# Optimization experiments

Measured on AMD Instinct MI355X. Metric: run time of the kernel, lower is better.

The kernel has to match this reference:

```python
import jax, jax.numpy as jnp
import numpy as np

B, C, H, W = 16, 512, 32, 32
G = 32            # GroupNorm groups (hard-coded in Normalize)
EPS = 1e-6
TEXT = 180        # text_ch
F = H * W         # in_features, asserted H*W == in_features


def setup_inputs() -> dict:
    key = jax.random.key(0)
    ks = jax.random.split(key, 10)
    s = 0.02
    return {
        "x": jax.random.normal(ks[0], (B, C, H, W), dtype=jnp.float32),
        "condition": jax.random.normal(ks[1], (B, TEXT), dtype=jnp.float32),
        "gamma": jnp.ones((C,), dtype=jnp.float32),
        "beta": jnp.zeros((C,), dtype=jnp.float32),
        "wq": jax.random.normal(ks[2], (C, C), dtype=jnp.float32) * s,   # 1x1 conv [out,in]
        "bq": jax.random.normal(ks[3], (C,), dtype=jnp.float32) * s,
        "wk": jax.random.normal(ks[4], (F, TEXT), dtype=jnp.float32) * s,  # Linear(text_ch -> in_features)
        "bk": jax.random.normal(ks[5], (F,), dtype=jnp.float32) * s,
        "wv": jax.random.normal(ks[6], (F, TEXT), dtype=jnp.float32) * s,
        "bv": jax.random.normal(ks[7], (F,), dtype=jnp.float32) * s,
        "wo": jax.random.normal(ks[8], (C, C), dtype=jnp.float32) * s,   # proj_out 1x1 conv
        "bo": jax.random.normal(ks[9], (C,), dtype=jnp.float32) * s,
    }


def _group_norm(x, gamma, beta):
    b, c, h, w = x.shape
    xg = x.reshape(b, G, c // G, h, w)
    mu = xg.mean(axis=(2, 3, 4), keepdims=True)
    var = xg.var(axis=(2, 3, 4), keepdims=True)
    xn = ((xg - mu) * jax.lax.rsqrt(var + EPS)).reshape(b, c, h, w)
    return xn * gamma[None, :, None, None] + beta[None, :, None, None]


def reference(x, condition, gamma, beta, wq, bq, wk, bk, wv, bv, wo, bo):
    h_ = _group_norm(x, gamma, beta)                       # [B,C,H,W]
    # q: 1x1 conv
    q = jnp.einsum('bchw,oc->bohw', h_, wq) + bq[None, :, None, None]
    # condition.reshape(B,1,-1).repeat(1,C,1)
    cond = jnp.broadcast_to(condition[:, None, :], (B, C, TEXT))  # [B,C,T]
    k = jnp.einsum('bct,ft->bcf', cond, wk) + bk           # [B,C,F]
    v = jnp.einsum('bct,ft->bcf', cond, wv) + bv           # [B,C,F]
    q3 = q.reshape(B, C, H * W).transpose(0, 2, 1)         # [B,N,C], N=HW
    scale = C ** (-0.5)
    attn = jax.nn.softmax(jnp.einsum('bnc,bcf->bnf', q3, k) * scale, axis=2)  # [B,N,F]
    h2 = jnp.einsum('bcf,bnf->bcn', v, attn).reshape(B, C, H, W)
    out = jnp.einsum('bchw,oc->bohw', h2, wo) + bo[None, :, None, None]
    return x + out
```

## Files before the change

### kernel.cpp

```cpp
#include <hip/hip_runtime.h>

#define B_   16
#define C_   512
#define N_   1024
#define F_   1024
#define T_   180
#define G_   32

#define WS_MU    0
#define WS_RSIG  512
#define WS_K     1024
#define WS_V     (1024 + 16384)
#define WS_WQS   (1024 + 2*16384)
#define WS_WOS   (WS_WQS + 512)
#define WS_BQS   (WS_WOS + 512)
#define WS_POFF  (WS_BQS + 4)
#define WS_P     36864

__global__ __launch_bounds__(256) void k_w(
    const float* __restrict__ cond,
    const float* __restrict__ wq, const float* __restrict__ bq,
    const float* __restrict__ wk, const float* __restrict__ bk,
    const float* __restrict__ wv, const float* __restrict__ bv,
    const float* __restrict__ wo, float* __restrict__ ws)
{
    const int blk = blockIdx.x;
    const int tid = threadIdx.x;

    if (blk < 16) {
        const int c0 = blk << 5;
        const int oi = tid >> 5;
        const int ci = tid & 31;
        float acc = 0.f;
        #pragma unroll 8
        for (int ob = 0; ob < 64; ++ob) {
            const int o = (ob << 3) + oi;
            acc += wq[o * C_ + c0 + ci];
        }
        __shared__ float part[8][32];
        part[oi][ci] = acc;
        __syncthreads();
        if (tid < 32) {
            float s = 0.f;
            #pragma unroll
            for (int j = 0; j < 8; ++j) s += part[j][tid];
            ws[WS_WQS + c0 + tid] = s;
        }
    } else if (blk < 32) {
        const int o0 = (blk - 16) << 5;
        const int r  = tid >> 3;
        const int j  = tid & 7;
        const float4* row = (const float4*)(wo + (size_t)(o0 + r) * C_);
        float acc = 0.f;
        #pragma unroll
        for (int jj = 0; jj < 16; ++jj) {
            float4 p = row[(jj << 3) + j];
            acc += (p.x + p.y) + (p.z + p.w);
        }
        #pragma unroll
        for (int off = 4; off; off >>= 1) acc += __shfl_down(acc, off, 8);
        if (j == 0) ws[WS_WOS + o0 + r] = acc;
    } else if (blk < 96) {
        const int idx = blk - 32;
        const int b   = idx >> 2;
        const int f   = ((idx & 3) << 8) + tid;
        __shared__ __align__(16) float condl[T_];
        if (tid < T_) condl[tid] = cond[b * T_ + tid];
        __syncthreads();
        const float4* c4  = (const float4*)condl;
        const float4* wk4 = (const float4*)(wk + (size_t)f * T_);
        const float4* wv4 = (const float4*)(wv + (size_t)f * T_);
        float accK = bk[f];
        float accV = bv[f];
        #pragma unroll 5
        for (int t4 = 0; t4 < 45; ++t4) {
            float4 cf = c4[t4];
            float4 a  = wk4[t4];
            float4 vv = wv4[t4];
            accK = fmaf(cf.x, a.x,  fmaf(cf.y, a.y,  fmaf(cf.z, a.z,  fmaf(cf.w, a.w,  accK))));
            accV = fmaf(cf.x, vv.x, fmaf(cf.y, vv.y, fmaf(cf.z, vv.z, fmaf(cf.w, vv.w, accV))));
        }
        ws[WS_K + b * F_ + f] = accK;
        ws[WS_V + b * F_ + f] = accV;
    } else {
        float p = bq[tid] + bq[tid + 256];
        #pragma unroll
        for (int off = 32; off; off >>= 1) p += __shfl_down(p, off, 64);
        __shared__ float rb[4];
        if ((tid & 63) == 0) rb[tid >> 6] = p;
        __syncthreads();
        if (tid == 0) ws[WS_BQS] = rb[0] + rb[1] + rb[2] + rb[3];
    }
}

__global__ __launch_bounds__(256) void k_stats(
    const float* __restrict__ x, const float* __restrict__ gamma,
    const float* __restrict__ beta, float* __restrict__ ws)
{
    const int blk = blockIdx.x;
    const int g   = blk & 31;
    const int tid = threadIdx.x;

    __shared__ float wl[16], bwl[16];
    __shared__ float rs[4], rq[4];
    if (tid < 16) {
        const int c = (g << 4) + tid;
        const float wqs = ws[WS_WQS + c];
        wl[tid]  = gamma[c] * wqs;
        bwl[tid] = beta[c]  * wqs;
    }
    __syncthreads();

    const float4* xv = (const float4*)(x + (size_t)blk * 16384);
    float4 p4 = make_float4(0.f, 0.f, 0.f, 0.f);
    float s = 0.f, sq = 0.f;
    #pragma unroll
    for (int j = 0; j < 16; ++j) {
        float4 p = xv[tid + (j << 8)];
        s  += (p.x + p.y) + (p.z + p.w);
        sq += p.x * p.x + p.y * p.y + p.z * p.z + p.w * p.w;
        const float wj = wl[j];
        p4.x = fmaf(p.x, wj, p4.x);
        p4.y = fmaf(p.y, wj, p4.y);
        p4.z = fmaf(p.z, wj, p4.z);
        p4.w = fmaf(p.w, wj, p4.w);
    }
    *(float4*)(ws + WS_P + (size_t)blk * 1024 + (tid << 2)) = p4;

    #pragma unroll
    for (int off = 32; off; off >>= 1) {
        s  += __shfl_down(s,  off, 64);
        sq += __shfl_down(sq, off, 64);
    }
    if ((tid & 63) == 0) { rs[tid >> 6] = s; rq[tid >> 6] = sq; }
    __syncthreads();
    if (tid == 0) {
        const float S1 = rs[0] + rs[1] + rs[2] + rs[3];
        const float S2 = rq[0] + rq[1] + rq[2] + rq[3];
        const float mu  = S1 * (1.f / 16384.f);
        const float var = S2 * (1.f / 16384.f) - mu * mu;
        const float rsig = rsqrtf(var + 1e-6f);
        ws[WS_MU   + blk] = mu;
        ws[WS_RSIG + blk] = rsig;
        float sw = 0.f, sbw = 0.f;
        #pragma unroll
        for (int j = 0; j < 16; ++j) { sw += wl[j]; sbw += bwl[j]; }
        ws[WS_POFF + blk] = sbw - mu * rsig * sw;
    }
}

__global__ __launch_bounds__(256) void k_fused(
    const float* __restrict__ x, const float* __restrict__ bo,
    const float* __restrict__ ws, float* __restrict__ out)
{
    const int b   = blockIdx.x >> 5;
    const int n0  = (blockIdx.x & 31) << 5;
    const int tid = threadIdx.x;

    __shared__ __align__(16) float KV[2 * F_];
    __shared__ float rsigl[32];
    __shared__ float part[8][32];
    __shared__ float pse[8][32], psv[8][32];
    __shared__ float Sl[32], Al[32];
    __shared__ float redmx[4], redmn[4];
    __shared__ float opw;

    if (tid < 32) rsigl[tid] = ws[WS_RSIG + (b << 5) + tid];
    float op = (tid < 32) ? ws[WS_POFF + (b << 5) + tid] : 0.f;

    const float* Kg = ws + WS_K + b * F_;
    const float* Vg = ws + WS_V + b * F_;
    float mx = -1e30f, mn = 1e30f;
    float2* KV2 = (float2*)KV;
    #pragma unroll
    for (int i = tid; i < F_; i += 256) {
        float kv = Kg[i];
        KV2[i] = make_float2(kv, Vg[i]);
        mx = fmaxf(mx, kv);
        mn = fminf(mn, kv);
    }
    #pragma unroll
    for (int off = 32; off; off >>= 1) {
        op += __shfl_down(op, off, 64);
        mx = fmaxf(mx, __shfl_down(mx, off, 64));
        mn = fminf(mn, __shfl_down(mn, off, 64));
    }
    if ((tid & 63) == 0) {
        redmx[tid >> 6] = mx;
        redmn[tid >> 6] = mn;
        if (tid == 0) opw = op + ws[WS_BQS];
    }
    __syncthreads();
    const float offset = opw;
    const float maxK = fmaxf(fmaxf(redmx[0], redmx[1]), fmaxf(redmx[2], redmx[3]));
    const float minK = fminf(fminf(redmn[0], redmn[1]), fminf(redmn[2], redmn[3]));

    const int nl = tid & 31;
    const int gq = tid >> 5;
    {
        const float* Pp = ws + WS_P + ((size_t)((b << 5) + (gq << 2)) << 10) + n0 + nl;
        float acc = 0.f;
        #pragma unroll
        for (int j = 0; j < 4; ++j)
            acc = fmaf(rsigl[(gq << 2) + j], Pp[(size_t)j << 10], acc);
        part[gq][nl] = acc;
    }
    __syncthreads();
    if (tid < 32) {
        float s8 = 0.f;
        #pragma unroll
        for (int j = 0; j < 8; ++j) s8 += part[j][tid];
        Sl[tid] = s8 + offset;
    }
    __syncthreads();

    const float LOG2E = 1.4426950408889634f;
    const float scale = 0.044194173824159216f;
    const float s  = Sl[nl] * scale;
    const float sl = s * LOG2E;
    const float ml = (s >= 0.f ? maxK : minK) * sl;

    float se = 0.f, sv = 0.f;
    const int fq = tid >> 5;
    const int fbase = fq << 7;
    #pragma unroll 8
    for (int fi = 0; fi < 128; ++fi) {
        float2 kv = KV2[fbase + fi];
        float e = exp2f(fmaf(sl, kv.x, -ml));
        se += e;
        sv = fmaf(kv.y, e, sv);
    }
    pse[fq][nl] = se;
    psv[fq][nl] = sv;

    const int col = tid & 7;
    const int row = tid >> 3;
    const float* WOS = ws + WS_WOS;
    float wv_[16], bo_[16];
    #pragma unroll
    for (int p = 0; p < 16; ++p) {
        wv_[p] = WOS[(p << 5) + row];
        bo_[p] = bo[(p << 5) + row];
    }

    __syncthreads();
    if (tid < 32) {
        float den = 0.f, num = 0.f;
        #pragma unroll
        for (int j = 0; j < 8; ++j) { den += pse[j][tid]; num += psv[j][tid]; }
        Al[tid] = num / den;
    }
    __syncthreads();

    float av[4];
    #pragma unroll
    for (int j = 0; j < 4; ++j) av[j] = Al[(col << 2) + j];

    #pragma unroll
    for (int p = 0; p < 16; ++p) {
        const int o = (p << 5) + row;
        const size_t base = (((size_t)(b * C_ + o)) << 10) + n0 + (col << 2);
        float4 xv = *(const float4*)(x + base);
        float4 ov;
        ov.x = xv.x + fmaf(av[0], wv_[p], bo_[p]);
        ov.y = xv.y + fmaf(av[1], wv_[p], bo_[p]);
        ov.z = xv.z + fmaf(av[2], wv_[p], bo_[p]);
        ov.w = xv.w + fmaf(av[3], wv_[p], bo_[p]);
        *(float4*)(out + base) = ov;
    }
}

extern "C" void kernel_launch(void* const* d_in, const int* in_sizes, int n_in,
                              void* d_out, int out_size, void* d_ws, size_t ws_size,
                              hipStream_t stream) {
    const float* x     = (const float*)d_in[0];
    const float* cond  = (const float*)d_in[1];
    const float* gamma = (const float*)d_in[2];
    const float* beta  = (const float*)d_in[3];
    const float* wq    = (const float*)d_in[4];
    const float* bq    = (const float*)d_in[5];
    const float* wk    = (const float*)d_in[6];
    const float* bk    = (const float*)d_in[7];
    const float* wv    = (const float*)d_in[8];
    const float* bv    = (const float*)d_in[9];
    const float* wo    = (const float*)d_in[10];
    const float* bo    = (const float*)d_in[11];
    float* ws  = (float*)d_ws;
    float* out = (float*)d_out;

    hipLaunchKernelGGL(k_w, dim3(97), dim3(256), 0, stream,
                       cond, wq, bq, wk, bk, wv, bv, wo, ws);
    hipLaunchKernelGGL(k_stats, dim3(512), dim3(256), 0, stream,
                       x, gamma, beta, ws);
    hipLaunchKernelGGL(k_fused, dim3(512), dim3(256), 0, stream,
                       x, bo, ws, out);
}
```

Baseline: 125.9 us.

## Split fused attention kernel into attention-scalar kernel and streaming output kernel

The fused kernel is split in two. k_attn computes the per-position attention scalar A and writes it to workspace. A new k_out kernel then does the x + A*wo + bo residual as a grid-stride float4 stream over 2048 blocks. The aim is to decouple the memory-bound output pass from the exp-heavy attention part, giving better occupancy and coalesced streaming. In exchange it adds a kernel launch and a small workspace round-trip, and moves the WS_P offset.

```diff
diff --git a/kernel.cpp b/kernel.cpp
--- a/kernel.cpp
+++ b/kernel.cpp
@@ -15,7 +15,8 @@
 #define WS_WOS   (WS_WQS + 512)
 #define WS_BQS   (WS_WOS + 512)
 #define WS_POFF  (WS_BQS + 4)
-#define WS_P     36864
+#define WS_A     (WS_POFF + 512)
+#define WS_P     65536
 
 __global__ __launch_bounds__(256) void k_w(
     const float* __restrict__ cond,
@@ -149,10 +150,10 @@
     }
 }
 
-__global__ __launch_bounds__(256) void k_fused(
-    const float* __restrict__ x, const float* __restrict__ bo,
-    const float* __restrict__ ws, float* __restrict__ out)
-{
+__global__ __launch_bounds__(256) void k_attn(
+    const float* __restrict__ ws_in, float* __restrict__ ws)
+{
+    const float* wsr = ws_in;
     const int b   = blockIdx.x >> 5;
     const int n0  = (blockIdx.x & 31) << 5;
     const int tid = threadIdx.x;
@@ -161,15 +162,15 @@
     __shared__ float rsigl[32];
     __shared__ float part[8][32];
     __shared__ float pse[8][32], psv[8][32];
-    __shared__ float Sl[32], Al[32];
+    __shared__ float Sl[32];
     __shared__ float redmx[4], redmn[4];
     __shared__ float opw;
 
-    if (tid < 32) rsigl[tid] = ws[WS_RSIG + (b << 5) + tid];
-    float op = (tid < 32) ? ws[WS_POFF + (b << 5) + tid] : 0.f;
-
-    const float* Kg = ws + WS_K + b * F_;
-    const float* Vg = ws + WS_V + b * F_;
+    if (tid < 32) rsigl[tid] = wsr[WS_RSIG + (b << 5) + tid];
+    float op = (tid < 32) ? wsr[WS_POFF + (b << 5) + tid] : 0.f;
+
+    const float* Kg = wsr + WS_K + b * F_;
+    const float* Vg = wsr + WS_V + b * F_;
     float mx = -1e30f, mn = 1e30f;
     float2* KV2 = (float2*)KV;
     #pragma unroll
@@ -188,7 +189,7 @@
     if ((tid & 63) == 0) {
         redmx[tid >> 6] = mx;
         redmn[tid >> 6] = mn;
-        if (tid == 0) opw = op + ws[WS_BQS];
+        if (tid == 0) opw = op + wsr[WS_BQS];
     }
     __syncthreads();
     const float offset = opw;
@@ -198,7 +199,7 @@
     const int nl = tid & 31;
     const int gq = tid >> 5;
     {
-        const float* Pp = ws + WS_P + ((size_t)((b << 5) + (gq << 2)) << 10) + n0 + nl;
+        const float* Pp = wsr + WS_P + ((size_t)((b << 5) + (gq << 2)) << 10) + n0 + nl;
         float acc = 0.f;
         #pragma unroll
         for (int j = 0; j < 4; ++j)
@@ -232,41 +233,37 @@
     }
     pse[fq][nl] = se;
     psv[fq][nl] = sv;
-
-    const int col = tid & 7;
-    const int row = tid >> 3;
-    const float* WOS = ws + WS_WOS;
-    float wv_[16], bo_[16];
-    #pragma unroll
-    for (int p = 0; p < 16; ++p) {
-        wv_[p] = WOS[(p << 5) + row];
-        bo_[p] = bo[(p << 5) + row];
-    }
-
     __syncthreads();
     if (tid < 32) {
         float den = 0.f, num = 0.f;
         #pragma unroll
         for (int j = 0; j < 8; ++j) { den += pse[j][tid]; num += psv[j][tid]; }
-        Al[tid] = num / den;
-    }
-    __syncthreads();
-
-    float av[4];
-    #pragma unroll
-    for (int j = 0; j < 4; ++j) av[j] = Al[(col << 2) + j];
-
-    #pragma unroll
-    for (int p = 0; p < 16; ++p) {
-        const int o = (p << 5) + row;
-        const size_t base = (((size_t)(b * C_ + o)) << 10) + n0 + (col << 2);
-        float4 xv = *(const float4*)(x + base);
+        ws[WS_A + (b << 10) + n0 + tid] = num / den;
+    }
+}
+
+__global__ __launch_bounds__(256) void k_out(
+    const float* __restrict__ x, const float* __restrict__ bo,
+    const float* __restrict__ ws, float* __restrict__ out)
+{
+    const int tot4 = B_ * C_ * (N_ / 4);
+    const int stride = 2048 * 256;
+    int i4 = blockIdx.x * 256 + threadIdx.x;
+    #pragma unroll 4
+    for (int it = 0; it < 4; ++it, i4 += stride) {
+        const int n4 = i4 & 255;
+        const int o  = (i4 >> 8) & 511;
+        const int b  = i4 >> 17;
+        const float4 a4 = *(const float4*)(ws + WS_A + (b << 10) + (n4 << 2));
+        const float w   = ws[WS_WOS + o];
+        const float bof = bo[o];
+        const float4 xv = ((const float4*)x)[i4];
         float4 ov;
-        ov.x = xv.x + fmaf(av[0], wv_[p], bo_[p]);
-        ov.y = xv.y + fmaf(av[1], wv_[p], bo_[p]);
-        ov.z = xv.z + fmaf(av[2], wv_[p], bo_[p]);
-        ov.w = xv.w + fmaf(av[3], wv_[p], bo_[p]);
-        *(float4*)(out + base) = ov;
+        ov.x = xv.x + fmaf(a4.x, w, bof);
+        ov.y = xv.y + fmaf(a4.y, w, bof);
+        ov.z = xv.z + fmaf(a4.z, w, bof);
+        ov.w = xv.w + fmaf(a4.w, w, bof);
+        ((float4*)out)[i4] = ov;
     }
 }
 
@@ -292,6 +289,8 @@
                        cond, wq, bq, wk, bk, wv, bv, wo, ws);
     hipLaunchKernelGGL(k_stats, dim3(512), dim3(256), 0, stream,
                        x, gamma, beta, ws);
-    hipLaunchKernelGGL(k_fused, dim3(512), dim3(256), 0, stream,
+    hipLaunchKernelGGL(k_attn, dim3(512), dim3(256), 0, stream,
+                       ws, ws);
+    hipLaunchKernelGGL(k_out, dim3(2048), dim3(256), 0, stream,
                        x, bo, ws, out);
 }
```

Result: slower. 131.7 us (+4.6%).

## Merge weight-prep and group-stats kernels into one prep kernel

Applied to the files above, without the earlier changes.

Fuses the weight-reduction kernel and the GroupNorm statistics kernel into a single launch. Each stats block now recomputes the wq column sums for its own 16 channels instead of reading them from a prior kernel, and it issues its x loads into registers before that reduction so the two overlap. This removes one kernel launch and the dependency gap between the two. In exchange, the wq column-sum work is repeated across the 16 batches, and register pressure rises from holding 16 float4 values per thread.

```diff
diff --git a/kernel.cpp b/kernel.cpp
--- a/kernel.cpp
+++ b/kernel.cpp
@@ -11,14 +11,14 @@
 #define WS_RSIG  512
 #define WS_K     1024
 #define WS_V     (1024 + 16384)
-#define WS_WQS   (1024 + 2*16384)
-#define WS_WOS   (WS_WQS + 512)
+#define WS_WOS   (1024 + 2*16384)
 #define WS_BQS   (WS_WOS + 512)
 #define WS_POFF  (WS_BQS + 4)
 #define WS_P     36864
 
-__global__ __launch_bounds__(256) void k_w(
-    const float* __restrict__ cond,
+__global__ __launch_bounds__(256) void k_prep(
+    const float* __restrict__ x, const float* __restrict__ gamma,
+    const float* __restrict__ beta, const float* __restrict__ cond,
     const float* __restrict__ wq, const float* __restrict__ bq,
     const float* __restrict__ wk, const float* __restrict__ bk,
     const float* __restrict__ wv, const float* __restrict__ bv,
@@ -27,41 +27,76 @@
     const int blk = blockIdx.x;
     const int tid = threadIdx.x;
 
-    if (blk < 16) {
-        const int c0 = blk << 5;
-        const int oi = tid >> 5;
-        const int ci = tid & 31;
-        float acc = 0.f;
-        #pragma unroll 8
-        for (int ob = 0; ob < 64; ++ob) {
-            const int o = (ob << 3) + oi;
-            acc += wq[o * C_ + c0 + ci];
-        }
-        __shared__ float part[8][32];
-        part[oi][ci] = acc;
-        __syncthreads();
-        if (tid < 32) {
-            float s = 0.f;
+    if (blk < 512) {
+        const int g  = blk & 31;
+        const int c0 = g << 4;
+
+        const float4* xv = (const float4*)(x + (size_t)blk * 16384);
+        float4 xr[16];
+        #pragma unroll
+        for (int j = 0; j < 16; ++j) xr[j] = xv[tid + (j << 8)];
+
+        __shared__ float wqpart[16][16];
+        {
+            const int j  = tid & 15;
+            const int oi = tid >> 4;
+            const float* wqp = wq + (size_t)oi * C_ + c0 + j;
+            float a = 0.f;
+            #pragma unroll 8
+            for (int k = 0; k < 32; ++k)
+                a += wqp[(size_t)(k << 4) * C_];
+            wqpart[oi][j] = a;
+        }
+        __syncthreads();
+        __shared__ float wl[16], bwl[16];
+        if (tid < 16) {
+            float wqs = 0.f;
             #pragma unroll
-            for (int j = 0; j < 8; ++j) s += part[j][tid];
-            ws[WS_WQS + c0 + tid] = s;
-        }
-    } else if (blk < 32) {
-        const int o0 = (blk - 16) << 5;
-        const int r  = tid >> 3;
-        const int j  = tid & 7;
-        const float4* row = (const float4*)(wo + (size_t)(o0 + r) * C_);
-        float acc = 0.f;
-        #pragma unroll
-        for (int jj = 0; jj < 16; ++jj) {
-            float4 p = row[(jj << 3) + j];
-            acc += (p.x + p.y) + (p.z + p.w);
-        }
-        #pragma unroll
-        for (int off = 4; off; off >>= 1) acc += __shfl_down(acc, off, 8);
-        if (j == 0) ws[WS_WOS + o0 + r] = acc;
-    } else if (blk < 96) {
-        const int idx = blk - 32;
+            for (int k = 0; k < 16; ++k) wqs += wqpart[k][tid];
+            const int c = c0 + tid;
+            wl[tid]  = gamma[c] * wqs;
+            bwl[tid] = beta[c]  * wqs;
+        }
+        __syncthreads();
+
+        float4 p4 = make_float4(0.f, 0.f, 0.f, 0.f);
+        float s = 0.f, sq = 0.f;
+        #pragma unroll
+        for (int j = 0; j < 16; ++j) {
+            float4 p = xr[j];
+            s  += (p.x + p.y) + (p.z + p.w);
+            sq += p.x * p.x + p.y * p.y + p.z * p.z + p.w * p.w;
+            const float wj = wl[j];
+            p4.x = fmaf(p.x, wj, p4.x);
+            p4.y = fmaf(p.y, wj, p4.y);
+            p4.z = fmaf(p.z, wj, p4.z);
+            p4.w = fmaf(p.w, wj, p4.w);
+        }
+        *(float4*)(ws + WS_P + (size_t)blk * 1024 + (tid << 2)) = p4;
+
+        __shared__ float rs[4], rq[4];
+        #pragma unroll
+        for (int off = 32; off; off >>= 1) {
+            s  += __shfl_down(s,  off, 64);
+            sq += __shfl_down(sq, off, 64);
+        }
+        if ((tid & 63) == 0) { rs[tid >> 6] = s; rq[tid >> 6] = sq; }
+        __syncthreads();
+        if (tid == 0) {
+            const float S1 = rs[0] + rs[1] + rs[2] + rs[3];
+            const float S2 = rq[0] + rq[1] + rq[2] + rq[3];
+            const float mu  = S1 * (1.f / 16384.f);
+            const float var = S2 * (1.f / 16384.f) - mu * mu;
+            const float rsig = rsqrtf(var + 1e-6f);
+            ws[WS_MU   + blk] = mu;
+            ws[WS_RSIG + blk] = rsig;
+            float sw = 0.f, sbw = 0.f;
+            #pragma unroll
+            for (int j = 0; j < 16; ++j) { sw += wl[j]; sbw += bwl[j]; }
+            ws[WS_POFF + blk] = sbw - mu * rsig * sw;
+        }
+    } else if (blk < 576) {
+        const int idx = blk - 512;
         const int b   = idx >> 2;
         const int f   = ((idx & 3) << 8) + tid;
         __shared__ __align__(16) float condl[T_];
@@ -82,6 +117,20 @@
         }
         ws[WS_K + b * F_ + f] = accK;
         ws[WS_V + b * F_ + f] = accV;
+    } else if (blk < 592) {
+        const int o0 = (blk - 576) << 5;
+        const int r  = tid >> 3;
+        const int j  = tid & 7;
+        const float4* row = (const float4*)(wo + (size_t)(o0 + r) * C_);
+        float acc = 0.f;
+        #pragma unroll
+        for (int jj = 0; jj < 16; ++jj) {
+            float4 p = row[(jj << 3) + j];
+            acc += (p.x + p.y) + (p.z + p.w);
+        }
+        #pragma unroll
+        for (int off = 4; off; off >>= 1) acc += __shfl_down(acc, off, 8);
+        if (j == 0) ws[WS_WOS + o0 + r] = acc;
     } else {
         float p = bq[tid] + bq[tid + 256];
         #pragma unroll
@@ -90,62 +139,6 @@
         if ((tid & 63) == 0) rb[tid >> 6] = p;
         __syncthreads();
         if (tid == 0) ws[WS_BQS] = rb[0] + rb[1] + rb[2] + rb[3];
-    }
-}
-
-__global__ __launch_bounds__(256) void k_stats(
-    const float* __restrict__ x, const float* __restrict__ gamma,
-    const float* __restrict__ beta, float* __restrict__ ws)
-{
-    const int blk = blockIdx.x;
-    const int g   = blk & 31;
-    const int tid = threadIdx.x;
-
-    __shared__ float wl[16], bwl[16];
-    __shared__ float rs[4], rq[4];
-    if (tid < 16) {
-        const int c = (g << 4) + tid;
-        const float wqs = ws[WS_WQS + c];
-        wl[tid]  = gamma[c] * wqs;
-        bwl[tid] = beta[c]  * wqs;
-    }
-    __syncthreads();
-
-    const float4* xv = (const float4*)(x + (size_t)blk * 16384);
-    float4 p4 = make_float4(0.f, 0.f, 0.f, 0.f);
-    float s = 0.f, sq = 0.f;
-    #pragma unroll
-    for (int j = 0; j < 16; ++j) {
-        float4 p = xv[tid + (j << 8)];
-        s  += (p.x + p.y) + (p.z + p.w);
-        sq += p.x * p.x + p.y * p.y + p.z * p.z + p.w * p.w;
-        const float wj = wl[j];
-        p4.x = fmaf(p.x, wj, p4.x);
-        p4.y = fmaf(p.y, wj, p4.y);
-        p4.z = fmaf(p.z, wj, p4.z);
-        p4.w = fmaf(p.w, wj, p4.w);
-    }
-    *(float4*)(ws + WS_P + (size_t)blk * 1024 + (tid << 2)) = p4;
-
-    #pragma unroll
-    for (int off = 32; off; off >>= 1) {
-        s  += __shfl_down(s,  off, 64);
-        sq += __shfl_down(sq, off, 64);
-    }
-    if ((tid & 63) == 0) { rs[tid >> 6] = s; rq[tid >> 6] = sq; }
-    __syncthreads();
-    if (tid == 0) {
-        const float S1 = rs[0] + rs[1] + rs[2] + rs[3];
-        const float S2 = rq[0] + rq[1] + rq[2] + rq[3];
-        const float mu  = S1 * (1.f / 16384.f);
-        const float var = S2 * (1.f / 16384.f) - mu * mu;
-        const float rsig = rsqrtf(var + 1e-6f);
-        ws[WS_MU   + blk] = mu;
-        ws[WS_RSIG + blk] = rsig;
-        float sw = 0.f, sbw = 0.f;
-        #pragma unroll
-        for (int j = 0; j < 16; ++j) { sw += wl[j]; sbw += bwl[j]; }
-        ws[WS_POFF + blk] = sbw - mu * rsig * sw;
     }
 }
 
@@ -288,10 +281,8 @@
     float* ws  = (float*)d_ws;
     float* out = (float*)d_out;
 
-    hipLaunchKernelGGL(k_w, dim3(97), dim3(256), 0, stream,
-                       cond, wq, bq, wk, bk, wv, bv, wo, ws);
-    hipLaunchKernelGGL(k_stats, dim3(512), dim3(256), 0, stream,
-                       x, gamma, beta, ws);
+    hipLaunchKernelGGL(k_prep, dim3(593), dim3(256), 0, stream,
+                       x, gamma, beta, cond, wq, bq, wk, bk, wv, bv, wo, ws);
     hipLaunchKernelGGL(k_fused, dim3(512), dim3(256), 0, stream,
                        x, bo, ws, out);
 }
```

Result: no change. 124.8 us (-0.9%).
